# Kernel optimization log

Measured on AMD Instinct MI355X. Metric: run time of the kernel, lower is better.

## Reference

```python
import jax, jax.numpy as jnp
import numpy as np

D_MODEL = 2048
N_HEADS = 16
KV_HEADS = 4
HEAD_DIM = D_MODEL // N_HEADS            # 128
GROUP = N_HEADS // KV_HEADS              # 4
KV_WIDTH = KV_HEADS * HEAD_DIM           # 512
B, T = 2, 2048


def setup_inputs() -> dict:
    key = jax.random.key(0)
    ks = jax.random.split(key, 5)
    s = 0.02
    x = jax.random.normal(ks[0], (B, T, D_MODEL), dtype=jnp.float32)
    attn_mask = jnp.tril(jnp.ones((T, T), dtype=bool))  # causal
    qkv_w = jax.random.normal(ks[1], (D_MODEL, D_MODEL + 2 * KV_WIDTH), dtype=jnp.float32) * s
    qkv_b = jax.random.normal(ks[2], (D_MODEL + 2 * KV_WIDTH,), dtype=jnp.float32) * s
    proj_w = jax.random.normal(ks[3], (D_MODEL, D_MODEL), dtype=jnp.float32) * s
    proj_b = jax.random.normal(ks[4], (D_MODEL,), dtype=jnp.float32) * s
    return {"x": x, "attn_mask": attn_mask, "qkv_w": qkv_w, "qkv_b": qkv_b,
            "proj_w": proj_w, "proj_b": proj_b}


def reference(x, attn_mask, qkv_w, qkv_b, proj_w, proj_b):
    b, t, c = x.shape
    qkv = x @ qkv_w + qkv_b                               # [b,t,3072]
    q = qkv[..., :D_MODEL]
    k = qkv[..., D_MODEL:D_MODEL + KV_WIDTH]
    v = qkv[..., D_MODEL + KV_WIDTH:]
    # q: [b, kv_heads, group, t, d]; k,v: [b, kv_heads, t, d]
    q = q.reshape(b, t, KV_HEADS, GROUP, HEAD_DIM).transpose(0, 2, 3, 1, 4)
    k = k.reshape(b, t, KV_HEADS, HEAD_DIM).transpose(0, 2, 1, 3)
    v = v.reshape(b, t, KV_HEADS, HEAD_DIM).transpose(0, 2, 1, 3)
    scale = 1.0 / jnp.sqrt(jnp.asarray(HEAD_DIM, dtype=x.dtype))
    att = jnp.einsum('bkgtd,bksd->bkgts', q, k) * scale   # [b,kv,g,t,t]
    att = jnp.where(attn_mask, att, jnp.asarray(-jnp.inf, dtype=att.dtype))
    att = jax.nn.softmax(att, axis=-1)
    out = jnp.einsum('bkgts,bksd->bkgtd', att, v)         # [b,kv,g,t,d]
    out = out.transpose(0, 3, 1, 2, 4).reshape(b, t, c)
    return out @ proj_w + proj_b
```

## Files before the change

kernel.cpp:

```cpp
#include <hip/hip_runtime.h>
#include <cstdint>
#include <cstddef>

#define D_MODEL 2048
#define T_SEQ   2048
#define BATCH   2
#define N_HEADS 16
#define KV_HEADS 4
#define HEAD_DIM 128
#define QKV_N   3072
#define ROWS    (BATCH * T_SEQ)

typedef float  floatx4 __attribute__((ext_vector_type(4)));
typedef short  shortx8 __attribute__((ext_vector_type(8)));
typedef __bf16 bf16x8  __attribute__((ext_vector_type(8)));

typedef const void __attribute__((address_space(1))) gvoid_t;
typedef void __attribute__((address_space(3)))       svoid_t;

__device__ __forceinline__ floatx4 mfma16(shortx8 a, shortx8 b, floatx4 c) {
  return __builtin_amdgcn_mfma_f32_16x16x32_bf16(
      __builtin_bit_cast(bf16x8, a), __builtin_bit_cast(bf16x8, b), c, 0, 0, 0);
}

__device__ __forceinline__ unsigned short f2bf(float f) {
  union { float f; unsigned int u; } v; v.f = f;
  unsigned int u = v.u;
  u += 0x7fffu + ((u >> 16) & 1u);
  return (unsigned short)(u >> 16);
}

__device__ __forceinline__ unsigned short f2bf_hw(float f) {
  return __builtin_bit_cast(unsigned short, (__bf16)f);
}

__global__ __launch_bounds__(256) void prep_kernel(
    const float* __restrict__ x, unsigned short* __restrict__ x_bf,
    const float* __restrict__ qkv_w, unsigned short* __restrict__ qkvw_t,
    const float* __restrict__ proj_w, unsigned short* __restrict__ projw_t)
{
  __shared__ float tile[32][33];
  const int bid = blockIdx.x, tid = threadIdx.x;
  if (bid < 8192) {
    const int i = bid * 256 + tid;
    float4 v = ((const float4*)x)[i];
    ushort4 o;
    o.x = f2bf(v.x); o.y = f2bf(v.y); o.z = f2bf(v.z); o.w = f2bf(v.w);
    ((ushort4*)x_bf)[i] = o;
    return;
  }
  const float* W; unsigned short* Wt; int N, bx, by;
  if (bid < 14336) { const int v = bid - 8192;  W = qkv_w;  Wt = qkvw_t;  N = QKV_N;   bx = v % 96; by = v / 96; }
  else             { const int v = bid - 14336; W = proj_w; Wt = projw_t; N = D_MODEL; bx = v % 64; by = v / 64; }
  const int K = D_MODEL;
  const int n0 = bx * 32, k0 = by * 32;
  const int tx = tid & 31, ty = tid >> 5;
  #pragma unroll
  for (int i = 0; i < 32; i += 8)
    tile[ty + i][tx] = W[(size_t)(k0 + ty + i) * N + n0 + tx];
  __syncthreads();
  #pragma unroll
  for (int i = 0; i < 32; i += 8)
    Wt[(size_t)(n0 + ty + i) * K + k0 + tx] = f2bf(tile[tx][ty + i]);
}

template<int NB>
__global__ __launch_bounds__(512, 2) void gemm256(
    const unsigned short* __restrict__ A,
    const unsigned short* __restrict__ Bt,
    const float* __restrict__ bias,
    void* __restrict__ Cout,
    unsigned short* __restrict__ kst,
    unsigned short* __restrict__ vst,
    int M, int N, int K, int cmode)
{
  __shared__ __align__(16) unsigned short lds[32768 + NB * 16384];
  const int tid  = threadIdx.x;
  const int wave = tid >> 6, lane = tid & 63;
  const int quad = lane >> 4, l16 = lane & 15;
  const int wr = wave >> 2, wc = wave & 3;
  const int bm = blockIdx.y * 256, bn = blockIdx.x * (NB * 128);
  const int NT = K >> 6;

  const int r0 = tid >> 3;
  const int cx = (tid & 7) ^ (r0 & 7);
  const size_t K64 = (size_t)64 * K;
  const unsigned short* a_src = A  + (size_t)(bm + r0) * K + cx * 8;
  const unsigned short* b_src = Bt + (size_t)(bn + r0) * K + cx * 8;
  const int wOff = wave * 512;

  #define LDSA_(buf, half) (lds + (((buf) << 1) + (half)) * 8192)
  #define LDSB_(buf, half) (lds + 32768 + (((buf) << 1) + (half)) * (NB * 4096))
  #define KOFFA(h, t) ((size_t)(h) * 128 * K + (size_t)(t) * 64)
  #define KOFFB(h, t) ((size_t)(h) * (64 * NB) * K + (size_t)(t) * 64)
  #define STAGE_A(srcbase, ldshalf, koff) do {                                        \
    __builtin_amdgcn_global_load_lds((gvoid_t*)((srcbase) + (koff)),                  \
        (svoid_t*)((ldshalf) + wOff), 16, 0, 0);                                      \
    __builtin_amdgcn_global_load_lds((gvoid_t*)((srcbase) + (koff) + K64),            \
        (svoid_t*)((ldshalf) + wOff + 4096), 16, 0, 0);                               \
  } while (0)
  #define STAGE_B(srcbase, ldshalf, koff) do {                                        \
    _Pragma("unroll")                                                                 \
    for (int j_ = 0; j_ < NB; ++j_)                                                   \
      __builtin_amdgcn_global_load_lds(                                               \
          (gvoid_t*)((srcbase) + (koff) + (size_t)j_ * K64),                          \
          (svoid_t*)((ldshalf) + wOff + j_ * 4096), 16, 0, 0);                        \
  } while (0)

  const int rowA = (wr * 64 + l16) * 64;
  const int rowB = (wc * (16 * NB) + l16) * 64;
  const int xo0 = ((quad)     ^ (l16 & 7)) * 8;
  const int xo1 = ((4 + quad) ^ (l16 & 7)) * 8;

  floatx4 acc[8][2 * NB] = {};
  shortx8 Afr[4][2];
  shortx8 Bfr[2 * NB][2];

  STAGE_A(a_src, LDSA_(0, 0), KOFFA(0, 0));
  STAGE_B(b_src, LDSB_(0, 0), KOFFB(0, 0));
  STAGE_B(b_src, LDSB_(0, 1), KOFFB(1, 0));
  STAGE_A(a_src, LDSA_(0, 1), KOFFA(1, 0));
  if (NT > 1) {
    STAGE_A(a_src, LDSA_(1, 0), KOFFA(0, 1));
    STAGE_B(b_src, LDSB_(1, 0), KOFFB(0, 1));
    STAGE_B(b_src, LDSB_(1, 1), KOFFB(1, 1));
  }

  for (int t = 0; t < NT; ++t) {
    const int buf = t & 1;
    unsigned short* sA0 = LDSA_(buf, 0);
    unsigned short* sA1 = LDSA_(buf, 1);
    unsigned short* sB0 = LDSB_(buf, 0);
    unsigned short* sB1 = LDSB_(buf, 1);

    if (t == NT - 1) asm volatile("s_waitcnt vmcnt(0)" ::: "memory");
    else if constexpr (NB == 2) asm volatile("s_waitcnt vmcnt(6)" ::: "memory");
    else                        asm volatile("s_waitcnt vmcnt(4)" ::: "memory");
    __builtin_amdgcn_s_barrier();
    #pragma unroll
    for (int mi = 0; mi < 4; ++mi) {
      Afr[mi][0] = *(const shortx8*)(sA0 + rowA + mi * 1024 + xo0);
      Afr[mi][1] = *(const shortx8*)(sA0 + rowA + mi * 1024 + xo1);
    }
    #pragma unroll
    for (int ni = 0; ni < NB; ++ni) {
      Bfr[ni][0] = *(const shortx8*)(sB0 + rowB + ni * 1024 + xo0);
      Bfr[ni][1] = *(const shortx8*)(sB0 + rowB + ni * 1024 + xo1);
    }
    if (t + 1 < NT) STAGE_A(a_src, LDSA_(buf ^ 1, 1), KOFFA(1, t + 1));
    asm volatile("s_waitcnt lgkmcnt(0)" ::: "memory");
    __builtin_amdgcn_s_setprio(1);
    #pragma unroll
    for (int ks = 0; ks < 2; ++ks)
      #pragma unroll
      for (int mi = 0; mi < 4; ++mi)
        #pragma unroll
        for (int ni = 0; ni < NB; ++ni)
          acc[mi][ni] = mfma16(Afr[mi][ks], Bfr[ni][ks], acc[mi][ni]);
    __builtin_amdgcn_s_setprio(0);
    __builtin_amdgcn_s_barrier();

    #pragma unroll
    for (int ni = 0; ni < NB; ++ni) {
      Bfr[NB + ni][0] = *(const shortx8*)(sB1 + rowB + ni * 1024 + xo0);
      Bfr[NB + ni][1] = *(const shortx8*)(sB1 + rowB + ni * 1024 + xo1);
    }
    if (t + 2 < NT) STAGE_A(a_src, LDSA_(buf, 0), KOFFA(0, t + 2));
    __builtin_amdgcn_s_barrier();
    asm volatile("s_waitcnt lgkmcnt(0)" ::: "memory");
    __builtin_amdgcn_s_setprio(1);
    #pragma unroll
    for (int ks = 0; ks < 2; ++ks)
      #pragma unroll
      for (int mi = 0; mi < 4; ++mi)
        #pragma unroll
        for (int ni = 0; ni < NB; ++ni)
          acc[mi][NB + ni] = mfma16(Afr[mi][ks], Bfr[NB + ni][ks], acc[mi][NB + ni]);
    __builtin_amdgcn_s_setprio(0);
    __builtin_amdgcn_s_barrier();

    #pragma unroll
    for (int mi = 0; mi < 4; ++mi) {
      Afr[mi][0] = *(const shortx8*)(sA1 + rowA + mi * 1024 + xo0);
      Afr[mi][1] = *(const shortx8*)(sA1 + rowA + mi * 1024 + xo1);
    }
    if (t + 2 < NT) STAGE_B(b_src, LDSB_(buf, 0), KOFFB(0, t + 2));
    __builtin_amdgcn_s_barrier();
    asm volatile("s_waitcnt lgkmcnt(0)" ::: "memory");
    __builtin_amdgcn_s_setprio(1);
    #pragma unroll
    for (int ks = 0; ks < 2; ++ks)
      #pragma unroll
      for (int mi = 0; mi < 4; ++mi)
        #pragma unroll
        for (int ni = 0; ni < NB; ++ni)
          acc[4 + mi][NB + ni] = mfma16(Afr[mi][ks], Bfr[NB + ni][ks], acc[4 + mi][NB + ni]);
    __builtin_amdgcn_s_setprio(0);
    __builtin_amdgcn_s_barrier();

    if (t + 2 < NT) STAGE_B(b_src, LDSB_(buf, 1), KOFFB(1, t + 2));
    __builtin_amdgcn_s_barrier();
    __builtin_amdgcn_s_setprio(1);
    #pragma unroll
    for (int ks = 0; ks < 2; ++ks)
      #pragma unroll
      for (int mi = 0; mi < 4; ++mi)
        #pragma unroll
        for (int ni = 0; ni < NB; ++ni)
          acc[4 + mi][ni] = mfma16(Afr[mi][ks], Bfr[ni][ks], acc[4 + mi][ni]);
    __builtin_amdgcn_s_setprio(0);
    __builtin_amdgcn_s_barrier();
  }

  #pragma unroll
  for (int mi = 0; mi < 8; ++mi) {
    const int row = bm + (mi >> 2) * 128 + wr * 64 + (mi & 3) * 16 + quad * 4;
    #pragma unroll
    for (int ni = 0; ni < 2 * NB; ++ni) {
      const int col = bn + (ni / NB) * (64 * NB) + wc * (16 * NB) + (ni % NB) * 16 + l16;
      const float bv = bias[col];
      #pragma unroll
      for (int r = 0; r < 4; ++r) {
        float v = acc[mi][ni][r] + bv;
        if (cmode == 0) {
          ((float*)Cout)[(size_t)(row + r) * N + col] = v;
        } else {
          const unsigned short h = f2bf_hw(v);
          const int rw = row + r;
          const int t = rw & 2047, bb = rw >> 11;
          if (col < 2048) {
            ((unsigned short*)Cout)[(size_t)rw * 2048 + col] = h;
          } else if (col < 2560) {
            const int c2 = col - 2048, kvh = c2 >> 7, d = c2 & 127;
            kst[((((size_t)bb * 4 + kvh) * 16 + (d >> 3)) * 2048 + t) * 8 + (d & 7)] = h;
          } else {
            const int c2 = col - 2560, kvh = c2 >> 7, d = c2 & 127;
            vst[((((size_t)bb * 4 + kvh) * 256 + (t >> 3)) * 128 + d) * 8 + (t & 7)] = h;
          }
        }
      }
    }
  }
  #undef LDSA_
  #undef LDSB_
  #undef KOFFA
  #undef KOFFB
  #undef STAGE_A
  #undef STAGE_B
}

__global__ __launch_bounds__(512, 4) void attn_kernel(
    const unsigned short* __restrict__ qbuf,
    const unsigned short* __restrict__ kst,
    const unsigned short* __restrict__ vst,
    unsigned short* __restrict__ aout)
{
  __shared__ __align__(16) unsigned short sK[2][16 * 64 * 8];
  __shared__ __align__(16) unsigned short sV[2][8 * 128 * 8];
  __shared__ __align__(16) unsigned short sP[8][4 * 16 * 8];

  const int tid  = threadIdx.x;
  const int wave = tid >> 6, lane = tid & 63;
  const int split = wave >> 2, g = wave & 3;
  const int quad = lane >> 4, l16 = lane & 15;
  const int head = blockIdx.y, b = blockIdx.z;
  const int kvh = head >> 2;
  const float cf = 0.08838834764831845f * 1.4426950408889634f;
  const float THR = 25.0f;

  const unsigned short* kbase = kst + (size_t)((b * KV_HEADS + kvh) * 16) * 2048 * 8;
  const unsigned short* vbase = vst + (size_t)((b * KV_HEADS + kvh) * 256) * 128 * 8;
  unsigned short* sPw = sP[wave];

  float* mrgO  = (float*)&sK[0][0];
  float* mrgML = (float*)&sV[0][0];

  #define STAGE_KV(sp, kb_) do {                                               \
    _Pragma("unroll")                                                          \
    for (int it_ = 0; it_ < 4; ++it_) {                                        \
      const int c_ = it_ * 4 + g;                                              \
      __builtin_amdgcn_global_load_lds(                                        \
          (gvoid_t*)(kbase + ((size_t)c_ * 2048 + (kb_)) * 8 + lane * 8),      \
          (svoid_t*)(&sK[sp][c_ * 512]), 16, 0, 0);                            \
    }                                                                          \
    const unsigned short* vt_ = vbase + (size_t)((kb_) >> 3) * 128 * 8;        \
    _Pragma("unroll")                                                          \
    for (int it_ = 0; it_ < 4; ++it_) {                                        \
      const int c_ = it_ * 4 + g;                                              \
      __builtin_amdgcn_global_load_lds(                                        \
          (gvoid_t*)(vt_ + c_ * 512 + lane * 8),                               \
          (svoid_t*)(&sV[sp][c_ * 512]), 16, 0, 0);                            \
    }                                                                          \
  } while (0)

  #pragma unroll 1
  for (int half = 0; half < 2; ++half) {
    const int qt = half ? blockIdx.x : (31 - blockIdx.x);
    const int q0 = qt * 64;

    shortx8 qf[4];
    {
      const unsigned short* qp = qbuf + (size_t)(b * T_SEQ + q0 + g * 16 + l16) * 2048
                                 + head * HEAD_DIM + quad * 8;
      #pragma unroll
      for (int ks = 0; ks < 4; ++ks)
        qf[ks] = *(const shortx8*)(qp + ks * 32);
    }

    float m_i[4], l_i[4];
    #pragma unroll
    for (int r = 0; r < 4; ++r) { m_i[r] = -__builtin_inff(); l_i[r] = 0.f; }
    floatx4 o_acc[8] = {};

    const int J = (qt >> 1) + 1;
    for (int j = 0; j < J; ++j) {
      const int kt = 2 * j + split;
      const bool act = (kt <= qt);
      floatx4 s[4] = {};

      __builtin_amdgcn_s_barrier();
      if (act) STAGE_KV(split, kt * 64);
      asm volatile("s_waitcnt vmcnt(4)" ::: "memory");
      __builtin_amdgcn_s_barrier();

      if (act) {
        __builtin_amdgcn_s_setprio(1);
        #pragma unroll
        for (int ks = 0; ks < 4; ++ks) {
          #pragma unroll
          for (int ct = 0; ct < 4; ++ct) {
            shortx8 kf = *(const shortx8*)&sK[split][((ks * 4 + quad) * 64 + ct * 16 + l16) * 8];
            s[ct] = mfma16(qf[ks], kf, s[ct]);
          }
        }
        __builtin_amdgcn_s_setprio(0);

        if (kt == qt) {
          const int qrow = q0 + g * 16 + quad * 4;
          const int kb = kt * 64;
          #pragma unroll
          for (int ct = 0; ct < 4; ++ct) {
            const int kcol = kb + ct * 16 + l16;
            #pragma unroll
            for (int r = 0; r < 4; ++r)
              if (kcol > qrow + r) s[ct][r] = -__builtin_inff();
          }
        }

        float lmx[4];
        bool over = false;
        #pragma unroll
        for (int r = 0; r < 4; ++r) {
          lmx[r] = fmaxf(fmaxf(s[0][r], s[1][r]), fmaxf(s[2][r], s[3][r]));
          over = over || (lmx[r] > m_i[r] + THR);
        }
        if (__ballot(over)) {
          float alpha_r[4];
          #pragma unroll
          for (int r = 0; r < 4; ++r) {
            float m = lmx[r];
            m = fmaxf(m, __shfl_xor(m, 1));
            m = fmaxf(m, __shfl_xor(m, 2));
            m = fmaxf(m, __shfl_xor(m, 4));
            m = fmaxf(m, __shfl_xor(m, 8));
            const float newm = fmaxf(m_i[r], m);
            alpha_r[r] = exp2f((m_i[r] - newm) * cf);
            m_i[r] = newm;
            l_i[r] *= alpha_r[r];
          }
          #pragma unroll
          for (int nt = 0; nt < 8; ++nt)
            #pragma unroll
            for (int r = 0; r < 4; ++r) o_acc[nt][r] *= alpha_r[r];
        }

        #pragma unroll
        for (int r = 0; r < 4; ++r) {
          const float nmc = m_i[r] * cf;
          float p0 = exp2f(fmaf(s[0][r], cf, -nmc));
          float p1 = exp2f(fmaf(s[1][r], cf, -nmc));
          float p2 = exp2f(fmaf(s[2][r], cf, -nmc));
          float p3 = exp2f(fmaf(s[3][r], cf, -nmc));
          s[0][r] = p0; s[1][r] = p1; s[2][r] = p2; s[3][r] = p3;
          l_i[r] += (p0 + p1) + (p2 + p3);
        }
      }

      asm volatile("s_waitcnt vmcnt(0)" ::: "memory");
      __builtin_amdgcn_s_barrier();

      if (act) {
        #pragma unroll
        for (int c = 0; c < 2; ++c) {
          #pragma unroll
          for (int ctl = 0; ctl < 2; ++ctl) {
            const int ct = c * 2 + ctl;
            #pragma unroll
            for (int r = 0; r < 4; ++r)
              sPw[((ctl * 2 + (l16 >> 3)) * 16 + quad * 4 + r) * 8 + (l16 & 7)] =
                  f2bf_hw(s[ct][r]);
          }
          __asm__ __volatile__("s_waitcnt lgkmcnt(0)" ::: "memory");
          shortx8 pf = *(const shortx8*)&sPw[(quad * 16 + l16) * 8];
          __builtin_amdgcn_s_setprio(1);
          #pragma unroll
          for (int nt = 0; nt < 8; ++nt) {
            shortx8 vf = *(const shortx8*)&sV[split][((c * 4 + quad) * 128 + nt * 16 + l16) * 8];
            o_acc[nt] = mfma16(pf, vf, o_acc[nt]);
          }
          __builtin_amdgcn_s_setprio(0);
        }
      }
    }

    __builtin_amdgcn_s_barrier();
    if (split == 1) {
      #pragma unroll
      for (int nt = 0; nt < 8; ++nt)
        #pragma unroll
        for (int r = 0; r < 4; ++r)
          mrgO[g * 2048 + (quad * 4 + r) * 128 + nt * 16 + l16] = o_acc[nt][r];
      #pragma unroll
      for (int r = 0; r < 4; ++r) {
        mrgML[(g * 64 + lane) * 8 + r * 2]     = m_i[r];
        mrgML[(g * 64 + lane) * 8 + r * 2 + 1] = l_i[r];
      }
    }
    asm volatile("s_waitcnt lgkmcnt(0)" ::: "memory");
    __builtin_amdgcn_s_barrier();

    if (split == 0) {
      float lm[4], a0[4], a1[4];
      #pragma unroll
      for (int r = 0; r < 4; ++r) {
        const float m1 = mrgML[(g * 64 + lane) * 8 + r * 2];
        const float l1 = mrgML[(g * 64 + lane) * 8 + r * 2 + 1];
        const float M = fmaxf(m_i[r], m1);
        a0[r] = exp2f((m_i[r] - M) * cf);
        a1[r] = exp2f((m1 - M) * cf);
        lm[r] = a0[r] * l_i[r] + a1[r] * l1;
      }
      #pragma unroll
      for (int nt = 0; nt < 8; ++nt)
        #pragma unroll
        for (int r = 0; r < 4; ++r)
          o_acc[nt][r] = a0[r] * o_acc[nt][r]
                       + a1[r] * mrgO[g * 2048 + (quad * 4 + r) * 128 + nt * 16 + l16];

      const int trow = q0 + g * 16 + quad * 4;
      #pragma unroll
      for (int r = 0; r < 4; ++r) {
        float l = lm[r];
        l += __shfl_xor(l, 1);
        l += __shfl_xor(l, 2);
        l += __shfl_xor(l, 4);
        l += __shfl_xor(l, 8);
        const float inv = 1.f / l;
        #pragma unroll
        for (int nt = 0; nt < 8; ++nt) {
          aout[(size_t)(b * T_SEQ + trow + r) * D_MODEL + head * HEAD_DIM + nt * 16 + l16] =
              f2bf_hw(o_acc[nt][r] * inv);
        }
      }
    }
  }
  #undef STAGE_KV
}

extern "C" void kernel_launch(void* const* d_in, const int* in_sizes, int n_in,
                              void* d_out, int out_size, void* d_ws, size_t ws_size,
                              hipStream_t stream) {
  const float* x      = (const float*)d_in[0];
  const float* qkv_w  = (const float*)d_in[2];
  const float* qkv_b  = (const float*)d_in[3];
  const float* proj_w = (const float*)d_in[4];
  const float* proj_b = (const float*)d_in[5];
  float* out = (float*)d_out;

  char* ws = (char*)d_ws;
  unsigned short* x_bf    = (unsigned short*)(ws);
  unsigned short* qkvw_t  = (unsigned short*)(ws + (size_t)16777216);
  unsigned short* projw_t = (unsigned short*)(ws + (size_t)29360128);
  unsigned short* qbuf    = (unsigned short*)(ws + (size_t)37748736);
  unsigned short* kstaged = (unsigned short*)(ws + (size_t)54525952);
  unsigned short* vstaged = (unsigned short*)(ws + (size_t)58720256);
  unsigned short* attn_out = x_bf;

  prep_kernel<<<18432, 256, 0, stream>>>(x, x_bf, qkv_w, qkvw_t, proj_w, projw_t);
  gemm256<2><<<dim3(QKV_N / 256, ROWS / 256), 512, 0, stream>>>(
      x_bf, qkvw_t, qkv_b, (void*)qbuf, kstaged, vstaged, ROWS, QKV_N, D_MODEL, 2);
  attn_kernel<<<dim3(16, N_HEADS, BATCH), 512, 0, stream>>>(qbuf, kstaged, vstaged, attn_out);
  gemm256<1><<<dim3(D_MODEL / 128, ROWS / 256), 512, 0, stream>>>(
      attn_out, projw_t, proj_b, (void*)out, nullptr, nullptr, ROWS, D_MODEL, D_MODEL, 0);
}
```

Before: 313.9 us.

## Compute transposed S in attention to feed P from registers, dropping LDS round-trip

Swaps the MFMA operand order so each lane holds one query row's scores across key columns. The P tile can then be packed to bf16 directly in registers and used as the B operand of the PV MFMA, with no LDS write/read. To match the register layout, the V store in the QKV GEMM epilogue permutes token order within 32-token groups. Softmax state drops to one scalar per lane, and row reductions become two cross-quad shuffles. The output is written as packed 8-byte stores. In exchange, the layout coupling between the GEMM epilogue and the attention kernel becomes more fragile.

```diff
diff --git a/kernel.cpp b/kernel.cpp
--- a/kernel.cpp
+++ b/kernel.cpp
@@ -32,6 +32,10 @@
 
 __device__ __forceinline__ unsigned short f2bf_hw(float f) {
   return __builtin_bit_cast(unsigned short, (__bf16)f);
+}
+
+__device__ __forceinline__ unsigned int pk2bf(float lo, float hi) {
+  return (unsigned int)f2bf_hw(lo) | ((unsigned int)f2bf_hw(hi) << 16);
 }
 
 __global__ __launch_bounds__(256) void prep_kernel(
@@ -235,7 +239,8 @@
             kst[((((size_t)bb * 4 + kvh) * 16 + (d >> 3)) * 2048 + t) * 8 + (d & 7)] = h;
           } else {
             const int c2 = col - 2560, kvh = c2 >> 7, d = c2 & 127;
-            vst[((((size_t)bb * 4 + kvh) * 256 + (t >> 3)) * 128 + d) * 8 + (t & 7)] = h;
+            const int ts = (t & ~31) | (((t >> 2) & 3) << 3) | (((t >> 4) & 1) << 2) | (t & 3);
+            vst[((((size_t)bb * 4 + kvh) * 256 + (ts >> 3)) * 128 + d) * 8 + (ts & 7)] = h;
           }
         }
       }
@@ -257,7 +262,6 @@
 {
   __shared__ __align__(16) unsigned short sK[2][16 * 64 * 8];
   __shared__ __align__(16) unsigned short sV[2][8 * 128 * 8];
-  __shared__ __align__(16) unsigned short sP[8][4 * 16 * 8];
 
   const int tid  = threadIdx.x;
   const int wave = tid >> 6, lane = tid & 63;
@@ -270,7 +274,6 @@
 
   const unsigned short* kbase = kst + (size_t)((b * KV_HEADS + kvh) * 16) * 2048 * 8;
   const unsigned short* vbase = vst + (size_t)((b * KV_HEADS + kvh) * 256) * 128 * 8;
-  unsigned short* sPw = sP[wave];
 
   float* mrgO  = (float*)&sK[0][0];
   float* mrgML = (float*)&sV[0][0];
@@ -307,16 +310,15 @@
         qf[ks] = *(const shortx8*)(qp + ks * 32);
     }
 
-    float m_i[4], l_i[4];
-    #pragma unroll
-    for (int r = 0; r < 4; ++r) { m_i[r] = -__builtin_inff(); l_i[r] = 0.f; }
+    float m_i = -__builtin_inff(), l_i = 0.f;
     floatx4 o_acc[8] = {};
 
     const int J = (qt >> 1) + 1;
     for (int j = 0; j < J; ++j) {
       const int kt = 2 * j + split;
       const bool act = (kt <= qt);
-      floatx4 s[4] = {};
+      floatx4 st[4] = {};
+      unsigned int pk[4][2];
 
       __builtin_amdgcn_s_barrier();
       if (act) STAGE_KV(split, kt * 64);
@@ -330,60 +332,53 @@
           #pragma unroll
           for (int ct = 0; ct < 4; ++ct) {
             shortx8 kf = *(const shortx8*)&sK[split][((ks * 4 + quad) * 64 + ct * 16 + l16) * 8];
-            s[ct] = mfma16(qf[ks], kf, s[ct]);
+            st[ct] = mfma16(kf, qf[ks], st[ct]);
           }
         }
         __builtin_amdgcn_s_setprio(0);
 
         if (kt == qt) {
-          const int qrow = q0 + g * 16 + quad * 4;
+          const int qrow = q0 + g * 16 + l16;
           const int kb = kt * 64;
           #pragma unroll
           for (int ct = 0; ct < 4; ++ct) {
-            const int kcol = kb + ct * 16 + l16;
             #pragma unroll
             for (int r = 0; r < 4; ++r)
-              if (kcol > qrow + r) s[ct][r] = -__builtin_inff();
+              if (kb + ct * 16 + quad * 4 + r > qrow) st[ct][r] = -__builtin_inff();
           }
         }
 
-        float lmx[4];
-        bool over = false;
-        #pragma unroll
-        for (int r = 0; r < 4; ++r) {
-          lmx[r] = fmaxf(fmaxf(s[0][r], s[1][r]), fmaxf(s[2][r], s[3][r]));
-          over = over || (lmx[r] > m_i[r] + THR);
-        }
-        if (__ballot(over)) {
-          float alpha_r[4];
-          #pragma unroll
-          for (int r = 0; r < 4; ++r) {
-            float m = lmx[r];
-            m = fmaxf(m, __shfl_xor(m, 1));
-            m = fmaxf(m, __shfl_xor(m, 2));
-            m = fmaxf(m, __shfl_xor(m, 4));
-            m = fmaxf(m, __shfl_xor(m, 8));
-            const float newm = fmaxf(m_i[r], m);
-            alpha_r[r] = exp2f((m_i[r] - newm) * cf);
-            m_i[r] = newm;
-            l_i[r] *= alpha_r[r];
-          }
+        float lmx = -__builtin_inff();
+        #pragma unroll
+        for (int ct = 0; ct < 4; ++ct)
+          lmx = fmaxf(lmx, fmaxf(fmaxf(st[ct][0], st[ct][1]), fmaxf(st[ct][2], st[ct][3])));
+        if (__ballot(lmx > m_i + THR)) {
+          float m = lmx;
+          m = fmaxf(m, __shfl_xor(m, 16));
+          m = fmaxf(m, __shfl_xor(m, 32));
+          const float newm = fmaxf(m_i, m);
+          const float alpha = exp2f((m_i - newm) * cf);
+          m_i = newm;
+          l_i *= alpha;
           #pragma unroll
           for (int nt = 0; nt < 8; ++nt)
             #pragma unroll
-            for (int r = 0; r < 4; ++r) o_acc[nt][r] *= alpha_r[r];
-        }
-
-        #pragma unroll
-        for (int r = 0; r < 4; ++r) {
-          const float nmc = m_i[r] * cf;
-          float p0 = exp2f(fmaf(s[0][r], cf, -nmc));
-          float p1 = exp2f(fmaf(s[1][r], cf, -nmc));
-          float p2 = exp2f(fmaf(s[2][r], cf, -nmc));
-          float p3 = exp2f(fmaf(s[3][r], cf, -nmc));
-          s[0][r] = p0; s[1][r] = p1; s[2][r] = p2; s[3][r] = p3;
-          l_i[r] += (p0 + p1) + (p2 + p3);
-        }
+            for (int r = 0; r < 4; ++r) o_acc[nt][r] *= alpha;
+        }
+
+        const float nmc = m_i * cf;
+        float ps = 0.f;
+        #pragma unroll
+        for (int ct = 0; ct < 4; ++ct) {
+          #pragma unroll
+          for (int r = 0; r < 4; ++r) {
+            st[ct][r] = exp2f(fmaf(st[ct][r], cf, -nmc));
+            ps += st[ct][r];
+          }
+          pk[ct][0] = pk2bf(st[ct][0], st[ct][1]);
+          pk[ct][1] = pk2bf(st[ct][2], st[ct][3]);
+        }
+        l_i += ps;
       }
 
       asm volatile("s_waitcnt vmcnt(0)" ::: "memory");
@@ -391,22 +386,15 @@
 
       if (act) {
         #pragma unroll
-        for (int c = 0; c < 2; ++c) {
-          #pragma unroll
-          for (int ctl = 0; ctl < 2; ++ctl) {
-            const int ct = c * 2 + ctl;
-            #pragma unroll
-            for (int r = 0; r < 4; ++r)
-              sPw[((ctl * 2 + (l16 >> 3)) * 16 + quad * 4 + r) * 8 + (l16 & 7)] =
-                  f2bf_hw(s[ct][r]);
-          }
-          __asm__ __volatile__("s_waitcnt lgkmcnt(0)" ::: "memory");
-          shortx8 pf = *(const shortx8*)&sPw[(quad * 16 + l16) * 8];
+        for (int kc = 0; kc < 2; ++kc) {
+          union { unsigned int u[4]; shortx8 s; } pa;
+          pa.u[0] = pk[2 * kc][0];     pa.u[1] = pk[2 * kc][1];
+          pa.u[2] = pk[2 * kc + 1][0]; pa.u[3] = pk[2 * kc + 1][1];
           __builtin_amdgcn_s_setprio(1);
           #pragma unroll
           for (int nt = 0; nt < 8; ++nt) {
-            shortx8 vf = *(const shortx8*)&sV[split][((c * 4 + quad) * 128 + nt * 16 + l16) * 8];
-            o_acc[nt] = mfma16(pf, vf, o_acc[nt]);
+            shortx8 vf = *(const shortx8*)&sV[split][((kc * 4 + quad) * 128 + nt * 16 + l16) * 8];
+            o_acc[nt] = mfma16(vf, pa.s, o_acc[nt]);
           }
           __builtin_amdgcn_s_setprio(0);
         }
@@ -419,48 +407,37 @@
       for (int nt = 0; nt < 8; ++nt)
         #pragma unroll
         for (int r = 0; r < 4; ++r)
-          mrgO[g * 2048 + (quad * 4 + r) * 128 + nt * 16 + l16] = o_acc[nt][r];
-      #pragma unroll
-      for (int r = 0; r < 4; ++r) {
-        mrgML[(g * 64 + lane) * 8 + r * 2]     = m_i[r];
-        mrgML[(g * 64 + lane) * 8 + r * 2 + 1] = l_i[r];
-      }
+          mrgO[g * 2048 + (nt * 16 + quad * 4 + r) * 16 + l16] = o_acc[nt][r];
+      mrgML[(g * 64 + lane) * 2]     = m_i;
+      mrgML[(g * 64 + lane) * 2 + 1] = l_i;
     }
     asm volatile("s_waitcnt lgkmcnt(0)" ::: "memory");
     __builtin_amdgcn_s_barrier();
 
     if (split == 0) {
-      float lm[4], a0[4], a1[4];
-      #pragma unroll
-      for (int r = 0; r < 4; ++r) {
-        const float m1 = mrgML[(g * 64 + lane) * 8 + r * 2];
-        const float l1 = mrgML[(g * 64 + lane) * 8 + r * 2 + 1];
-        const float M = fmaxf(m_i[r], m1);
-        a0[r] = exp2f((m_i[r] - M) * cf);
-        a1[r] = exp2f((m1 - M) * cf);
-        lm[r] = a0[r] * l_i[r] + a1[r] * l1;
-      }
+      const float m1 = mrgML[(g * 64 + lane) * 2];
+      const float l1 = mrgML[(g * 64 + lane) * 2 + 1];
+      const float M  = fmaxf(m_i, m1);
+      const float a0 = exp2f((m_i - M) * cf);
+      const float a1 = exp2f((m1 - M) * cf);
+      float lm = a0 * l_i + a1 * l1;
       #pragma unroll
       for (int nt = 0; nt < 8; ++nt)
         #pragma unroll
         for (int r = 0; r < 4; ++r)
-          o_acc[nt][r] = a0[r] * o_acc[nt][r]
-                       + a1[r] * mrgO[g * 2048 + (quad * 4 + r) * 128 + nt * 16 + l16];
-
-      const int trow = q0 + g * 16 + quad * 4;
-      #pragma unroll
-      for (int r = 0; r < 4; ++r) {
-        float l = lm[r];
-        l += __shfl_xor(l, 1);
-        l += __shfl_xor(l, 2);
-        l += __shfl_xor(l, 4);
-        l += __shfl_xor(l, 8);
-        const float inv = 1.f / l;
-        #pragma unroll
-        for (int nt = 0; nt < 8; ++nt) {
-          aout[(size_t)(b * T_SEQ + trow + r) * D_MODEL + head * HEAD_DIM + nt * 16 + l16] =
-              f2bf_hw(o_acc[nt][r] * inv);
-        }
+          o_acc[nt][r] = a0 * o_acc[nt][r]
+                       + a1 * mrgO[g * 2048 + (nt * 16 + quad * 4 + r) * 16 + l16];
+
+      lm += __shfl_xor(lm, 16);
+      lm += __shfl_xor(lm, 32);
+      const float inv = 1.f / lm;
+      const size_t orow = (size_t)(b * T_SEQ + q0 + g * 16 + l16) * D_MODEL + head * HEAD_DIM;
+      #pragma unroll
+      for (int nt = 0; nt < 8; ++nt) {
+        uint2 w;
+        w.x = pk2bf(o_acc[nt][0] * inv, o_acc[nt][1] * inv);
+        w.y = pk2bf(o_acc[nt][2] * inv, o_acc[nt][3] * inv);
+        *(uint2*)&aout[orow + nt * 16 + quad * 4] = w;
       }
     }
   }
```

New measurement: 293.3 us. 1.07x faster.
